# Performance work log

Hardware: AMD Instinct MI355X
Metric: run time of the kernel (lower is better)

The kernel has to match this reference:

```python
import jax, jax.numpy as jnp
import numpy as np

INIT_W = 10.0
INIT_B = -5.0
N, M, D = 2048, 10, 256


def setup_inputs() -> dict:
    key = jax.random.key(0)
    k1, = jax.random.split(key, 1)
    embeddings = jax.random.normal(k1, (N, M, D), dtype=jnp.float32)
    w = jnp.asarray(INIT_W, dtype=jnp.float32)
    b = jnp.asarray(INIT_B, dtype=jnp.float32)
    return {"embeddings": embeddings, "w": w, "b": b}


def _l2norm(x, axis=-1, eps=1e-12):
    # matches torch F.normalize: x / max(||x||, eps)
    n = jnp.sqrt(jnp.sum(x * x, axis=axis, keepdims=True))
    return x / jnp.maximum(n, eps)


def reference(embeddings, w, b):
    # embeddings: (N, M, D)
    centroids = _l2norm(embeddings.mean(axis=1))          # (N, D)
    emb_norm = _l2norm(embeddings)                        # (N, M, D)
    sim = jnp.einsum('nmd,kd->nmk', emb_norm, centroids)  # (N, M, N)
    sim = sim * jnp.abs(w) + b
    # cross-entropy with target n for every (n, m):
    # loss = mean_{n,m} [ logsumexp_k sim[n,m,k] - sim[n,m,n] ]
    lse = jax.nn.logsumexp(sim, axis=-1)                  # (N, M)
    pos = jnp.take_along_axis(
        sim, jnp.arange(sim.shape[0])[:, None, None], axis=-1
    )[..., 0]                                             # (N, M)
    return jnp.mean(lse - pos)
```

## Files before the change

kernel.cpp:

```cpp
#include <hip/hip_runtime.h>
#include <hip/hip_bf16.h>

#define N_SPK 2048
#define M_UTT 10
#define D_DIM 256
#define NM (N_SPK * M_UTT)

typedef __attribute__((ext_vector_type(8))) short bf16x8_t;
typedef __attribute__((ext_vector_type(16))) float f32x16_t;

__device__ __forceinline__ short f2bf(float x) {
  __hip_bfloat16 h = __float2bfloat16(x);
  return *reinterpret_cast<short*>(&h);
}

__global__ __launch_bounds__(256) void k_centroid(const float* __restrict__ emb,
                                                  float* __restrict__ cent_f,
                                                  __hip_bfloat16* __restrict__ Bf) {
  int n = blockIdx.x, d = threadIdx.x;
  const float* p = emb + (size_t)n * (M_UTT * D_DIM) + d;
  float s = 0.f;
#pragma unroll
  for (int m = 0; m < M_UTT; ++m) s += p[m * D_DIM];
  float ss = s * s;
#pragma unroll
  for (int o = 32; o >= 1; o >>= 1) ss += __shfl_xor(ss, o, 64);
  __shared__ float red[4];
  int wid = threadIdx.x >> 6, lane = threadIdx.x & 63;
  if (lane == 0) red[wid] = ss;
  __syncthreads();
  float tot = red[0] + red[1] + red[2] + red[3];
  float inv = 1.0f / fmaxf(sqrtf(tot), 1e-11f);
  float v = s * inv;
  cent_f[n * D_DIM + d] = v;
  int idx = (((n >> 5) * 16 + (d >> 4)) * 64 + ((d >> 3) & 1) * 32 + (n & 31)) * 8 + (d & 7);
  Bf[idx] = __float2bfloat16(v);
}

__global__ __launch_bounds__(256) void k_prep(const float* __restrict__ emb,
                                              const float* __restrict__ cent_f,
                                              __hip_bfloat16* __restrict__ embn,
                                              float* __restrict__ dvals,
                                              float* __restrict__ rowsum) {
  int wid = threadIdx.x >> 6, lane = threadIdx.x & 63;
  int g = blockIdx.x * 4 + wid;
  const float4 e = ((const float4*)(emb + (size_t)g * D_DIM))[lane];
  int n = g / M_UTT;
  const float4 c = ((const float4*)(cent_f + (size_t)n * D_DIM))[lane];
  float ss = e.x * e.x + e.y * e.y + e.z * e.z + e.w * e.w;
  float dt = e.x * c.x + e.y * c.y + e.z * c.z + e.w * c.w;
#pragma unroll
  for (int o = 32; o >= 1; o >>= 1) {
    ss += __shfl_xor(ss, o, 64);
    dt += __shfl_xor(dt, o, 64);
  }
  float rn = 1.0f / fmaxf(sqrtf(ss), 1e-12f);
  short4 v;
  v.x = f2bf(e.x * rn); v.y = f2bf(e.y * rn);
  v.z = f2bf(e.z * rn); v.w = f2bf(e.w * rn);
  ((short4*)embn)[(size_t)g * 64 + lane] = v;
  if (lane == 0) {
    dvals[g] = dt * rn;
    rowsum[g] = 0.f;
  }
}

__global__ __launch_bounds__(512, 2) void k_gemm(const __hip_bfloat16* __restrict__ embn,
                                                 const __hip_bfloat16* __restrict__ Bf,
                                                 float* __restrict__ rowsum,
                                                 const float* __restrict__ wp) {
  __shared__ short As[128 * 256];
  const float aw = fabsf(wp[0]);
  const int tid = threadIdx.x;
  const int lane = tid & 63, w = tid >> 6;
  const int l31 = lane & 31, lh = lane >> 5;
  const int row0 = blockIdx.x * 128;

  {
    const short* srcbase = (const short*)embn;
#pragma unroll
    for (int p = 0; p < 8; ++p) {
      int r = p * 16 + w * 2 + lh;
      const short* src = srcbase + (size_t)(row0 + r) * D_DIM + ((l31 ^ (r & 7)) << 3);
      __builtin_amdgcn_global_load_lds(
          (const __attribute__((address_space(1))) void*)src,
          (__attribute__((address_space(3))) void*)&As[p * 4096 + w * 512],
          16, 0, 0);
    }
  }
  asm volatile("s_waitcnt vmcnt(0)" ::: "memory");
  __syncthreads();

  const int cg = blockIdx.y * 16 + w * 2;
  const bf16x8_t* bp = (const bf16x8_t*)Bf;

  f32x16_t acc[4][2];
#pragma unroll
  for (int rg = 0; rg < 4; ++rg)
#pragma unroll
    for (int ci = 0; ci < 2; ++ci)
#pragma unroll
      for (int r = 0; r < 16; ++r) acc[rg][ci][r] = 0.f;

#pragma unroll
  for (int ks = 0; ks < 16; ++ks) {
    bf16x8_t b0 = bp[(size_t)(cg * 16 + ks) * 64 + lane];
    bf16x8_t b1 = bp[(size_t)((cg + 1) * 16 + ks) * 64 + lane];
    const int sw = ((ks * 2 + lh) ^ (l31 & 7)) << 3;
    bf16x8_t e0 = *(const bf16x8_t*)&As[l31 * 256 + sw];
    bf16x8_t e1 = *(const bf16x8_t*)&As[(l31 + 32) * 256 + sw];
    bf16x8_t e2 = *(const bf16x8_t*)&As[(l31 + 64) * 256 + sw];
    bf16x8_t e3 = *(const bf16x8_t*)&As[(l31 + 96) * 256 + sw];
    acc[0][0] = __builtin_amdgcn_mfma_f32_32x32x16_bf16(b0, e0, acc[0][0], 0, 0, 0);
    acc[0][1] = __builtin_amdgcn_mfma_f32_32x32x16_bf16(b1, e0, acc[0][1], 0, 0, 0);
    acc[1][0] = __builtin_amdgcn_mfma_f32_32x32x16_bf16(b0, e1, acc[1][0], 0, 0, 0);
    acc[1][1] = __builtin_amdgcn_mfma_f32_32x32x16_bf16(b1, e1, acc[1][1], 0, 0, 0);
    acc[2][0] = __builtin_amdgcn_mfma_f32_32x32x16_bf16(b0, e2, acc[2][0], 0, 0, 0);
    acc[2][1] = __builtin_amdgcn_mfma_f32_32x32x16_bf16(b1, e2, acc[2][1], 0, 0, 0);
    acc[3][0] = __builtin_amdgcn_mfma_f32_32x32x16_bf16(b0, e3, acc[3][0], 0, 0, 0);
    acc[3][1] = __builtin_amdgcn_mfma_f32_32x32x16_bf16(b1, e3, acc[3][1], 0, 0, 0);
  }

#pragma unroll
  for (int rg = 0; rg < 4; ++rg) {
    float s = 0.f;
#pragma unroll
    for (int ci = 0; ci < 2; ++ci)
#pragma unroll
      for (int r = 0; r < 16; ++r)
        s += __expf(fmaf(aw, acc[rg][ci][r], -aw));
    s += __shfl_xor(s, 32, 64);
    if (lane < 32) atomicAdd(&rowsum[row0 + rg * 32 + lane], s);
  }
}

__global__ __launch_bounds__(256) void k_final(const float* __restrict__ rowsum,
                                               const float* __restrict__ dvals,
                                               const float* __restrict__ wp,
                                               float* __restrict__ out) {
  float s = 0.f, ds = 0.f;
  for (int i = threadIdx.x; i < NM; i += 256) {
    s += logf(rowsum[i]);
    ds += dvals[i];
  }
#pragma unroll
  for (int o = 32; o >= 1; o >>= 1) {
    s += __shfl_xor(s, o, 64);
    ds += __shfl_xor(ds, o, 64);
  }
  __shared__ float rs[4], rd[4];
  int wid = threadIdx.x >> 6, lane = threadIdx.x & 63;
  if (lane == 0) { rs[wid] = s; rd[wid] = ds; }
  __syncthreads();
  if (threadIdx.x == 0) {
    float S = rs[0] + rs[1] + rs[2] + rs[3];
    float Dd = rd[0] + rd[1] + rd[2] + rd[3];
    float aw = fabsf(wp[0]);
    out[0] = S / (float)NM + aw * (1.0f - Dd / (float)NM);
  }
}

extern "C" void kernel_launch(void* const* d_in, const int* in_sizes, int n_in,
                              void* d_out, int out_size, void* d_ws, size_t ws_size,
                              hipStream_t stream) {
  const float* emb = (const float*)d_in[0];
  const float* wp  = (const float*)d_in[1];
  float* out = (float*)d_out;

  char* ws = (char*)d_ws;
  float* rowsum = (float*)(ws);
  float* dvals  = (float*)(ws + 131072);
  float* cent_f = (float*)(ws + 262144);
  __hip_bfloat16* Bf   = (__hip_bfloat16*)(ws + 2621440);
  __hip_bfloat16* embn = (__hip_bfloat16*)(ws + 4194304);

  k_centroid<<<N_SPK, 256, 0, stream>>>(emb, cent_f, Bf);
  k_prep<<<NM / 4, 256, 0, stream>>>(emb, cent_f, embn, dvals, rowsum);
  k_gemm<<<dim3(NM / 128, 4), 512, 0, stream>>>(embn, Bf, rowsum, wp);
  k_final<<<1, 256, 0, stream>>>(rowsum, dvals, wp, out);
}
```

Measured before the change: 126.5 us.

## Fuse centroid and prep kernels, prefetch GEMM operands, parallelize final reduction

Merges the centroid and normalization kernels into one per-speaker kernel, so embeddings are read once and the fp32 centroid buffer round trip and one launch go away. The GEMM loop now loads the next k-step's B fragments and LDS A fragments ahead of the current MFMAs, a software-pipelining step. The final reduction moves from one block to many blocks that atomically add into the output, which the prep kernel zeroes. The atomic float accumulation makes the summation order nondeterministic, and the prefetch raises register pressure.

```diff
diff --git a/kernel.cpp b/kernel.cpp
--- a/kernel.cpp
+++ b/kernel.cpp
@@ -14,55 +14,61 @@
   return *reinterpret_cast<short*>(&h);
 }
 
-__global__ __launch_bounds__(256) void k_centroid(const float* __restrict__ emb,
-                                                  float* __restrict__ cent_f,
-                                                  __hip_bfloat16* __restrict__ Bf) {
-  int n = blockIdx.x, d = threadIdx.x;
+__global__ __launch_bounds__(256) void k_prep(const float* __restrict__ emb,
+                                              __hip_bfloat16* __restrict__ Bf,
+                                              __hip_bfloat16* __restrict__ embn,
+                                              float* __restrict__ dvals,
+                                              float* __restrict__ rowsum,
+                                              float* __restrict__ out) {
+  const int n = blockIdx.x, d = threadIdx.x;
+  const int wid = d >> 6, lane = d & 63;
   const float* p = emb + (size_t)n * (M_UTT * D_DIM) + d;
+
+  float e[M_UTT];
   float s = 0.f;
 #pragma unroll
-  for (int m = 0; m < M_UTT; ++m) s += p[m * D_DIM];
+  for (int m = 0; m < M_UTT; ++m) { e[m] = p[m * D_DIM]; s += e[m]; }
+
   float ss = s * s;
 #pragma unroll
   for (int o = 32; o >= 1; o >>= 1) ss += __shfl_xor(ss, o, 64);
-  __shared__ float red[4];
-  int wid = threadIdx.x >> 6, lane = threadIdx.x & 63;
-  if (lane == 0) red[wid] = ss;
+  __shared__ float redc[4];
+  if (lane == 0) redc[wid] = ss;
   __syncthreads();
-  float tot = red[0] + red[1] + red[2] + red[3];
+  float tot = redc[0] + redc[1] + redc[2] + redc[3];
   float inv = 1.0f / fmaxf(sqrtf(tot), 1e-11f);
   float v = s * inv;
-  cent_f[n * D_DIM + d] = v;
+
   int idx = (((n >> 5) * 16 + (d >> 4)) * 64 + ((d >> 3) & 1) * 32 + (n & 31)) * 8 + (d & 7);
   Bf[idx] = __float2bfloat16(v);
-}
 
-__global__ __launch_bounds__(256) void k_prep(const float* __restrict__ emb,
-                                              const float* __restrict__ cent_f,
-                                              __hip_bfloat16* __restrict__ embn,
-                                              float* __restrict__ dvals,
-                                              float* __restrict__ rowsum) {
-  int wid = threadIdx.x >> 6, lane = threadIdx.x & 63;
-  int g = blockIdx.x * 4 + wid;
-  const float4 e = ((const float4*)(emb + (size_t)g * D_DIM))[lane];
-  int n = g / M_UTT;
-  const float4 c = ((const float4*)(cent_f + (size_t)n * D_DIM))[lane];
-  float ss = e.x * e.x + e.y * e.y + e.z * e.z + e.w * e.w;
-  float dt = e.x * c.x + e.y * c.y + e.z * c.z + e.w * c.w;
+  __shared__ float redm[M_UTT][2][4];
 #pragma unroll
-  for (int o = 32; o >= 1; o >>= 1) {
-    ss += __shfl_xor(ss, o, 64);
-    dt += __shfl_xor(dt, o, 64);
+  for (int m = 0; m < M_UTT; ++m) {
+    float a = e[m] * e[m], bb = e[m] * v;
+#pragma unroll
+    for (int o = 32; o >= 1; o >>= 1) {
+      a += __shfl_xor(a, o, 64);
+      bb += __shfl_xor(bb, o, 64);
+    }
+    if (lane == 0) { redm[m][0][wid] = a; redm[m][1][wid] = bb; }
   }
-  float rn = 1.0f / fmaxf(sqrtf(ss), 1e-12f);
-  short4 v;
-  v.x = f2bf(e.x * rn); v.y = f2bf(e.y * rn);
-  v.z = f2bf(e.z * rn); v.w = f2bf(e.w * rn);
-  ((short4*)embn)[(size_t)g * 64 + lane] = v;
-  if (lane == 0) {
-    dvals[g] = dt * rn;
-    rowsum[g] = 0.f;
+  __syncthreads();
+  __shared__ float rnb[M_UTT];
+  if (d < M_UTT) {
+    float ssm = redm[d][0][0] + redm[d][0][1] + redm[d][0][2] + redm[d][0][3];
+    float dtm = redm[d][1][0] + redm[d][1][1] + redm[d][1][2] + redm[d][1][3];
+    float rn = 1.0f / fmaxf(sqrtf(ssm), 1e-12f);
+    rnb[d] = rn;
+    dvals[n * M_UTT + d] = dtm * rn;
+    rowsum[n * M_UTT + d] = 0.f;
   }
+  if (n == 0 && d == 0) out[0] = 0.f;
+  __syncthreads();
+
+  short* eo = (short*)embn + (size_t)n * (M_UTT * D_DIM) + d;
+#pragma unroll
+  for (int m = 0; m < M_UTT; ++m) eo[m * D_DIM] = f2bf(e[m] * rnb[m]);
 }
 
 __global__ __launch_bounds__(512, 2) void k_gemm(const __hip_bfloat16* __restrict__ embn,
@@ -92,7 +98,8 @@
   __syncthreads();
 
   const int cg = blockIdx.y * 16 + w * 2;
-  const bf16x8_t* bp = (const bf16x8_t*)Bf;
+  const bf16x8_t* b0p = (const bf16x8_t*)Bf + (size_t)(cg * 16) * 64 + lane;
+  const bf16x8_t* b1p = (const bf16x8_t*)Bf + (size_t)((cg + 1) * 16) * 64 + lane;
 
   f32x16_t acc[4][2];
 #pragma unroll
@@ -102,23 +109,38 @@
 #pragma unroll
       for (int r = 0; r < 16; ++r) acc[rg][ci][r] = 0.f;
 
+  bf16x8_t cb0 = b0p[0], cb1 = b1p[0];
+  bf16x8_t e0, e1, e2, e3;
+  {
+    const int sw = (lh ^ (l31 & 7)) << 3;
+    e0 = *(const bf16x8_t*)&As[l31 * 256 + sw];
+    e1 = *(const bf16x8_t*)&As[(l31 + 32) * 256 + sw];
+    e2 = *(const bf16x8_t*)&As[(l31 + 64) * 256 + sw];
+    e3 = *(const bf16x8_t*)&As[(l31 + 96) * 256 + sw];
+  }
+
 #pragma unroll
   for (int ks = 0; ks < 16; ++ks) {
-    bf16x8_t b0 = bp[(size_t)(cg * 16 + ks) * 64 + lane];
-    bf16x8_t b1 = bp[(size_t)((cg + 1) * 16 + ks) * 64 + lane];
-    const int sw = ((ks * 2 + lh) ^ (l31 & 7)) << 3;
-    bf16x8_t e0 = *(const bf16x8_t*)&As[l31 * 256 + sw];
-    bf16x8_t e1 = *(const bf16x8_t*)&As[(l31 + 32) * 256 + sw];
-    bf16x8_t e2 = *(const bf16x8_t*)&As[(l31 + 64) * 256 + sw];
-    bf16x8_t e3 = *(const bf16x8_t*)&As[(l31 + 96) * 256 + sw];
-    acc[0][0] = __builtin_amdgcn_mfma_f32_32x32x16_bf16(b0, e0, acc[0][0], 0, 0, 0);
-    acc[0][1] = __builtin_amdgcn_mfma_f32_32x32x16_bf16(b1, e0, acc[0][1], 0, 0, 0);
-    acc[1][0] = __builtin_amdgcn_mfma_f32_32x32x16_bf16(b0, e1, acc[1][0], 0, 0, 0);
-    acc[1][1] = __builtin_amdgcn_mfma_f32_32x32x16_bf16(b1, e1, acc[1][1], 0, 0, 0);
-    acc[2][0] = __builtin_amdgcn_mfma_f32_32x32x16_bf16(b0, e2, acc[2][0], 0, 0, 0);
-    acc[2][1] = __builtin_amdgcn_mfma_f32_32x32x16_bf16(b1, e2, acc[2][1], 0, 0, 0);
-    acc[3][0] = __builtin_amdgcn_mfma_f32_32x32x16_bf16(b0, e3, acc[3][0], 0, 0, 0);
-    acc[3][1] = __builtin_amdgcn_mfma_f32_32x32x16_bf16(b1, e3, acc[3][1], 0, 0, 0);
+    bf16x8_t nb0, nb1, f0, f1, f2, f3;
+    if (ks < 15) {
+      nb0 = b0p[(ks + 1) * 64];
+      nb1 = b1p[(ks + 1) * 64];
+      const int sw = (((ks + 1) * 2 + lh) ^ (l31 & 7)) << 3;
+      f0 = *(const bf16x8_t*)&As[l31 * 256 + sw];
+      f1 = *(const bf16x8_t*)&As[(l31 + 32) * 256 + sw];
+      f2 = *(const bf16x8_t*)&As[(l31 + 64) * 256 + sw];
+      f3 = *(const bf16x8_t*)&As[(l31 + 96) * 256 + sw];
+    }
+    acc[0][0] = __builtin_amdgcn_mfma_f32_32x32x16_bf16(cb0, e0, acc[0][0], 0, 0, 0);
+    acc[0][1] = __builtin_amdgcn_mfma_f32_32x32x16_bf16(cb1, e0, acc[0][1], 0, 0, 0);
+    acc[1][0] = __builtin_amdgcn_mfma_f32_32x32x16_bf16(cb0, e1, acc[1][0], 0, 0, 0);
+    acc[1][1] = __builtin_amdgcn_mfma_f32_32x32x16_bf16(cb1, e1, acc[1][1], 0, 0, 0);
+    acc[2][0] = __builtin_amdgcn_mfma_f32_32x32x16_bf16(cb0, e2, acc[2][0], 0, 0, 0);
+    acc[2][1] = __builtin_amdgcn_mfma_f32_32x32x16_bf16(cb1, e2, acc[2][1], 0, 0, 0);
+    acc[3][0] = __builtin_amdgcn_mfma_f32_32x32x16_bf16(cb0, e3, acc[3][0], 0, 0, 0);
+    acc[3][1] = __builtin_amdgcn_mfma_f32_32x32x16_bf16(cb1, e3, acc[3][1], 0, 0, 0);
+    cb0 = nb0; cb1 = nb1;
+    e0 = f0; e1 = f1; e2 = f2; e3 = f3;
   }
 
 #pragma unroll
@@ -138,26 +160,22 @@
                                                const float* __restrict__ dvals,
                                                const float* __restrict__ wp,
                                                float* __restrict__ out) {
-  float s = 0.f, ds = 0.f;
-  for (int i = threadIdx.x; i < NM; i += 256) {
-    s += logf(rowsum[i]);
-    ds += dvals[i];
+  const float aw = fabsf(wp[0]);
+  int base = blockIdx.x * 512 + threadIdx.x;
+  float c = 0.f;
+#pragma unroll
+  for (int j = 0; j < 2; ++j) {
+    int r = base + j * 256;
+    c += logf(rowsum[r]) + aw * (1.0f - dvals[r]);
   }
 #pragma unroll
-  for (int o = 32; o >= 1; o >>= 1) {
-    s += __shfl_xor(s, o, 64);
-    ds += __shfl_xor(ds, o, 64);
-  }
-  __shared__ float rs[4], rd[4];
+  for (int o = 32; o >= 1; o >>= 1) c += __shfl_xor(c, o, 64);
+  __shared__ float rs[4];
   int wid = threadIdx.x >> 6, lane = threadIdx.x & 63;
-  if (lane == 0) { rs[wid] = s; rd[wid] = ds; }
+  if (lane == 0) rs[wid] = c;
   __syncthreads();
-  if (threadIdx.x == 0) {
-    float S = rs[0] + rs[1] + rs[2] + rs[3];
-    float Dd = rd[0] + rd[1] + rd[2] + rd[3];
-    float aw = fabsf(wp[0]);
-    out[0] = S / (float)NM + aw * (1.0f - Dd / (float)NM);
-  }
+  if (threadIdx.x == 0)
+    atomicAdd(out, (rs[0] + rs[1] + rs[2] + rs[3]) * (1.0f / (float)NM));
 }
 
 extern "C" void kernel_launch(void* const* d_in, const int* in_sizes, int n_in,
@@ -169,13 +187,11 @@
 
   char* ws = (char*)d_ws;
   float* rowsum = (float*)(ws);
-  float* dvals  = (float*)(ws + 131072);
-  float* cent_f = (float*)(ws + 262144);
-  __hip_bfloat16* Bf   = (__hip_bfloat16*)(ws + 2621440);
-  __hip_bfloat16* embn = (__hip_bfloat16*)(ws + 4194304);
+  float* dvals  = (float*)(ws + (128 << 10));
+  __hip_bfloat16* Bf   = (__hip_bfloat16*)(ws + (1 << 20));
+  __hip_bfloat16* embn = (__hip_bfloat16*)(ws + (2 << 20));
 
-  k_centroid<<<N_SPK, 256, 0, stream>>>(emb, cent_f, Bf);
-  k_prep<<<NM / 4, 256, 0, stream>>>(emb, cent_f, embn, dvals, rowsum);
+  k_prep<<<N_SPK, 256, 0, stream>>>(emb, Bf, embn, dvals, rowsum, out);
   k_gemm<<<dim3(NM / 128, 4), 512, 0, stream>>>(embn, Bf, rowsum, wp);
-  k_final<<<1, 256, 0, stream>>>(rowsum, dvals, wp, out);
+  k_final<<<NM / 512, 256, 0, stream>>>(rowsum, dvals, wp, out);
 }
```

Result: faster. 110.0 us (-13.0%).
